# Kernel tuning notes

Measured on AMD Instinct MI355X. Metric: run time of the kernel, lower is better.

The kernel has to match this reference:

```python
import jax, jax.numpy as jnp
import numpy as np

NSAMPLE = 16
BN_EPS = 1e-5


def setup_inputs() -> dict:
    key = jax.random.key(0)
    k1, k2, k3, k4, k5, k6 = jax.random.split(key, 6)
    B, N, Cin, Cout = 8, 8192, 64, 128
    xyz = jax.random.normal(k1, (B, N, 3), dtype=jnp.float32)
    feature = jax.random.normal(k2, (B, N, Cin), dtype=jnp.float32)
    W = jax.random.normal(k3, (Cin, Cout), dtype=jnp.float32) * 0.05
    b = jax.random.normal(k4, (Cout,), dtype=jnp.float32) * 0.01
    gamma = 1.0 + 0.1 * jax.random.normal(k5, (Cout,), dtype=jnp.float32)
    beta = 0.1 * jax.random.normal(k6, (Cout,), dtype=jnp.float32)
    return {"xyz": xyz, "feature": feature, "W": W, "b": b,
            "gamma": gamma, "beta": beta, "npoint": 2048}


def farthest_point_sample(xyz, npoint):
    # xyz: [B, N, 3] -> centroids: [B, npoint] int32
    B, N, _ = xyz.shape
    dist0 = jnp.full((B, N), 1e10, dtype=xyz.dtype)
    far0 = jnp.zeros((B,), dtype=jnp.int32)  # deterministic seed point (torch uses randint)

    def step(carry, _):
        distance, farthest = carry
        centroid = jnp.take_along_axis(xyz, farthest[:, None, None], axis=1)  # [B,1,3]
        d = jnp.sum((xyz - centroid) ** 2, axis=-1)  # [B,N]
        distance = jnp.minimum(distance, d)
        new_far = jnp.argmax(distance, axis=-1).astype(jnp.int32)
        return (distance, new_far), farthest

    (_, _), cents = jax.lax.scan(step, (dist0, far0), None, length=npoint)
    return cents.T  # [B, npoint]


def index_points(points, idx):
    # points: [B, N, C]; idx: [B, ...] -> [B, ..., C]
    B = points.shape[0]
    C = points.shape[-1]
    flat = idx.reshape(B, -1)
    out = jnp.take_along_axis(points, flat[..., None], axis=1)  # [B, M, C]
    return out.reshape(idx.shape + (C,))


def knn_point(nsample, xyz, new_xyz):
    # squared distances [B, npoint, N], then nsample smallest
    sqr = (-2.0 * jnp.einsum('bmc,bnc->bmn', new_xyz, xyz)
           + jnp.sum(new_xyz ** 2, -1)[..., None]
           + jnp.sum(xyz ** 2, -1)[:, None, :])
    _, idx = jax.lax.top_k(-sqr, nsample)
    return idx  # [B, npoint, nsample]


def reference(xyz, feature, W, b, gamma, beta, npoint):
    B = xyz.shape[0]
    new_xyz_idx = farthest_point_sample(xyz, npoint)          # [B, npoint]
    new_xyz = index_points(xyz, new_xyz_idx)                  # [B, npoint, 3]
    idx = knn_point(NSAMPLE, xyz, new_xyz)                    # [B, npoint, K]
    grouped_feature = index_points(feature, idx)              # [B, npoint, K, Cin]

    # pointwise MLP: Linear -> BatchNorm (batch stats, per out-channel) -> ReLU
    h = jnp.einsum('bnkc,cd->bnkd', grouped_feature, W) + b   # [B, npoint, K, Cout]
    mean = jnp.mean(h, axis=(0, 1, 2))
    var = jnp.mean((h - mean) ** 2, axis=(0, 1, 2))           # biased, as torch BN
    h = gamma * (h - mean) * jax.lax.rsqrt(var + BN_EPS) + beta
    h = jax.nn.relu(h)

    new_feature = jnp.max(h, axis=2)                          # [B, npoint, Cout]
    return new_xyz, new_feature
```

## Files before the change

kernel.cpp:

```cpp
#include <hip/hip_runtime.h>

typedef unsigned long long u64;
typedef unsigned int u32;
typedef float f32x2 __attribute__((ext_vector_type(2)));

constexpr int BATCH  = 8;
constexpr int NPTS   = 8192;
constexpr int CIN    = 64;
constexpr int COUT   = 128;
constexpr int NPOINT = 2048;
constexpr int KNN    = 16;

__global__ __launch_bounds__(256) void pp_kernel(const float* __restrict__ xyz,
                                                 float* __restrict__ pp) {
  int i = blockIdx.x * 256 + threadIdx.x;
  float x = xyz[i * 3 + 0], y = xyz[i * 3 + 1], z = xyz[i * 3 + 2];
  pp[i] = __fadd_rn(__fadd_rn(__fmul_rn(x, x), __fmul_rn(y, y)), __fmul_rn(z, z));
}

constexpr int FPS_T = 256;
constexpr int FPS_PAIRS = NPTS / FPS_T / 2;

#define DPP_LVL(CTRL)                                                          \
  {                                                                            \
    u32 hi_o = (u32)__builtin_amdgcn_update_dpp((int)khi, (int)khi, (CTRL),    \
                                                0xf, 0xf, false);              \
    u32 lo_o = (u32)__builtin_amdgcn_update_dpp((int)klo, (int)klo, (CTRL),    \
                                                0xf, 0xf, false);              \
    bool gt = (hi_o > khi) || ((hi_o == khi) && (lo_o > klo));                 \
    khi = gt ? hi_o : khi;                                                     \
    klo = gt ? lo_o : klo;                                                     \
  }

__global__ __launch_bounds__(256) void fps_kernel(const float* __restrict__ xyz,
                                                  float* __restrict__ out_xyz) {
#pragma clang fp contract(off)
  __shared__ float4 sP[NPTS];
  __shared__ u64 sKey[2][4];
  const int b = blockIdx.x;
  const int t = threadIdx.x;
  const int lane = t & 63;
  const int wv = t >> 6;
  const float* xb = xyz + (size_t)b * NPTS * 3;
  f32x2 px2[FPS_PAIRS], py2[FPS_PAIRS], pz2[FPS_PAIRS], pd2[FPS_PAIRS];
#pragma unroll
  for (int jp = 0; jp < FPS_PAIRS; ++jp) {
    int p0 = t + (2 * jp) * FPS_T;
    int p1 = t + (2 * jp + 1) * FPS_T;
    float x0 = xb[p0 * 3 + 0], y0 = xb[p0 * 3 + 1], z0 = xb[p0 * 3 + 2];
    float x1 = xb[p1 * 3 + 0], y1 = xb[p1 * 3 + 1], z1 = xb[p1 * 3 + 2];
    px2[jp] = (f32x2){x0, x1};
    py2[jp] = (f32x2){y0, y1};
    pz2[jp] = (f32x2){z0, z1};
    pd2[jp] = (f32x2){1e10f, 1e10f};
    sP[p0] = make_float4(x0, y0, z0, 0.f);
    sP[p1] = make_float4(x1, y1, z1, 0.f);
  }
  float cx = xb[0], cy = xb[1], cz = xb[2];
  float* outx = out_xyz + (size_t)b * NPOINT * 3;
  __syncthreads();
  for (int it = 0; it < NPOINT; ++it) {
    if (t == 0) {
      outx[it * 3 + 0] = cx; outx[it * 3 + 1] = cy; outx[it * 3 + 2] = cz;
    }
    const f32x2 cx2 = {cx, cx}, cy2 = {cy, cy}, cz2 = {cz, cz};
    float bd = -1.0f;
    int bj = 0;
#pragma unroll
    for (int jp = 0; jp < FPS_PAIRS; ++jp) {
      f32x2 dx = px2[jp] - cx2;
      f32x2 dy = py2[jp] - cy2;
      f32x2 dz = pz2[jp] - cz2;
      f32x2 d = (dx * dx + dy * dy) + dz * dz;
      f32x2 nd = __builtin_elementwise_min(pd2[jp], d);
      pd2[jp] = nd;
      if (nd.x > bd) { bd = nd.x; bj = 2 * jp; }
      if (nd.y > bd) { bd = nd.y; bj = 2 * jp + 1; }
    }
    const int bi0 = t + bj * FPS_T;
    u32 khi = __float_as_uint(bd);
    u32 klo = (u32)(8191 - bi0);
    DPP_LVL(0x111)
    DPP_LVL(0x112)
    DPP_LVL(0x114)
    DPP_LVL(0x118)
    DPP_LVL(0x142)
    DPP_LVL(0x143)
    const int par = it & 1;
    if (lane == 63) sKey[par][wv] = ((u64)khi << 32) | klo;
    __syncthreads();
    u64 k0 = sKey[par][0];
    u64 k1 = sKey[par][1];
    u64 k2 = sKey[par][2];
    u64 k3 = sKey[par][3];
    if (k1 > k0) k0 = k1;
    if (k3 > k2) k2 = k3;
    if (k2 > k0) k0 = k2;
    const int bi = 8191 - (int)(u32)(k0 & 0xFFFFFFFFu);
    float4 c4 = sP[bi];
    cx = c4.x; cy = c4.y; cz = c4.z;
  }
}

__global__ __launch_bounds__(512) void knn_kernel(const float* __restrict__ xyz,
                                                  const float* __restrict__ pp,
                                                  const float* __restrict__ new_xyz,
                                                  int* __restrict__ knn_idx) {
  __shared__ u64 smem[8192];
  const int tid = threadIdx.x;
  const int lane = tid & 63;
  const int wv = __builtin_amdgcn_readfirstlane(tid >> 6);
  const int bid = blockIdx.x;
  const int b = bid >> 5;
  const int qbase = (bid & 31) * 64;
  const int q = qbase + lane;
  const float* xb = xyz + (size_t)b * NPTS * 3;
  const float* ppb = pp + (size_t)b * NPTS;
  const float* nq = new_xyz + ((size_t)b * NPOINT + q) * 3;
  float qx = nq[0], qy = nq[1], qz = nq[2];
  float qq = __fadd_rn(__fadd_rn(__fmul_rn(qx, qx), __fmul_rn(qy, qy)),
                       __fmul_rn(qz, qz));

  u64 L[16];
#pragma unroll
  for (int s = 0; s < 16; ++s) L[s] = 0xFF800000FFFFFFFFULL;
  float cmax = __uint_as_float(0x7F800000u);
  int cnt = 0;

  auto flushfn = [&]() {
#pragma unroll
    for (int e = 0; e < 8; ++e) {
      if (e < cnt) {
        u64 key = smem[tid * 9 + e];
        if (key < L[15]) {
#pragma unroll
          for (int s = 15; s >= 1; --s)
            L[s] = (key < L[s - 1]) ? L[s - 1] : ((key < L[s]) ? key : L[s]);
          L[0] = (key < L[0]) ? key : L[0];
        }
      }
    }
    cnt = 0;
    u32 hb = (u32)(L[15] >> 32);
    hb ^= (hb >= 0x80000000u) ? 0x80000000u : 0xFFFFFFFFu;
    cmax = __uint_as_float(hb);
  };

  const int base = wv * 1024;
#pragma unroll 8
  for (int i = 0; i < 1024; ++i) {
    const int pidx = base + i;
    float ptx = xb[pidx * 3 + 0], pty = xb[pidx * 3 + 1], ptz = xb[pidx * 3 + 2];
    float pv = ppb[pidx];
    float dot = __fadd_rn(__fadd_rn(__fmul_rn(qx, ptx), __fmul_rn(qy, pty)),
                          __fmul_rn(qz, ptz));
    float d = __fadd_rn(__fadd_rn(__fmul_rn(-2.0f, dot), qq), pv);
    if (d <= cmax) {
      u32 xb32 = __float_as_uint(d);
      xb32 ^= ((int)xb32 < 0) ? 0xFFFFFFFFu : 0x80000000u;
      smem[tid * 9 + cnt] = ((u64)xb32 << 32) | (u32)pidx;
      ++cnt;
    }
    if (__any(cnt >= 8)) flushfn();
  }
  flushfn();
  __syncthreads();
#pragma unroll
  for (int s = 0; s < 16; ++s) smem[tid * 16 + s] = L[s];
  __syncthreads();
  if (tid < 64) {
    u64 h[8]; int pos[8];
#pragma unroll
    for (int w = 0; w < 8; ++w) { h[w] = smem[(w * 64 + tid) * 16]; pos[w] = 1; }
    int outv[16];
#pragma unroll
    for (int r = 0; r < 16; ++r) {
      u64 mv = h[0]; int mw = 0;
#pragma unroll
      for (int w = 1; w < 8; ++w) {
        if (h[w] < mv) { mv = h[w]; mw = w; }
      }
      outv[r] = (int)(mv & 0xFFFFFFFFULL);
#pragma unroll
      for (int w = 0; w < 8; ++w) {
        if (w == mw) {
          h[w] = (pos[w] < 16) ? smem[(w * 64 + tid) * 16 + pos[w]]
                               : 0xFFFFFFFFFFFFFFFFULL;
          pos[w]++;
        }
      }
    }
    int* dst = knn_idx + ((size_t)b * NPOINT + qbase + tid) * KNN;
#pragma unroll
    for (int r = 0; r < 16; r += 4)
      *(int4*)(dst + r) = make_int4(outv[r], outv[r + 1], outv[r + 2], outv[r + 3]);
  }
}

__global__ __launch_bounds__(256) void stats_kernel(const float* __restrict__ feature,
                                                    const float* __restrict__ Wm,
                                                    const float* __restrict__ bias,
                                                    const int* __restrict__ knn_idx,
                                                    double* __restrict__ stats) {
  __shared__ float s_part[256];
  const int tid = threadIdx.x;
  const int lane = tid & 63;
  const int wv = tid >> 6;
  const int tbase = blockIdx.x * 256 + tid;
  for (int chunk = 0; chunk < 4; ++chunk) {
    const int c0 = chunk * 32;
    float V[64];
#pragma unroll
    for (int j = 0; j < 64; ++j) V[j] = 0.f;
    for (int rr = 0; rr < 4; ++rr) {
      const int row = tbase + rr * 65536;
      const int bb = row >> 15;
      const int nbr = knn_idx[row];
      const float4* fp = (const float4*)(feature + ((size_t)bb * NPTS + nbr) * CIN);
      float acc[32];
#pragma unroll
      for (int j = 0; j < 32; ++j) acc[j] = bias[c0 + j];
      for (int cb = 0; cb < 8; ++cb) {
        float4 fa = fp[cb * 2 + 0], fb2 = fp[cb * 2 + 1];
        float fr[8] = {fa.x, fa.y, fa.z, fa.w, fb2.x, fb2.y, fb2.z, fb2.w};
#pragma unroll
        for (int cc = 0; cc < 8; ++cc) {
          const int c = cb * 8 + cc;
#pragma unroll
          for (int j = 0; j < 32; ++j)
            acc[j] = fmaf(fr[cc], Wm[c * COUT + c0 + j], acc[j]);
        }
      }
#pragma unroll
      for (int j = 0; j < 32; ++j) {
        V[j] += acc[j];
        V[32 + j] = fmaf(acc[j], acc[j], V[32 + j]);
      }
    }
#pragma unroll
    for (int o = 32; o >= 1; o >>= 1) {
      const bool hi = (lane & o) != 0;
#pragma unroll
      for (int j = 0; j < o; ++j) {
        float keep = hi ? V[o + j] : V[j];
        float send = hi ? V[j] : V[o + j];
        V[j] = keep + __shfl_xor(send, o);
      }
    }
    s_part[wv * 64 + lane] = V[0];
    __syncthreads();
    if (tid < 64) {
      float tot = s_part[tid] + s_part[64 + tid] + s_part[128 + tid] + s_part[192 + tid];
      int addr = (tid < 32) ? (c0 + tid) : (COUT + c0 + (tid - 32));
      atomicAdd(stats + addr, (double)tot);
    }
    __syncthreads();
  }
}

__global__ __launch_bounds__(256) void apply_kernel(const float* __restrict__ feature,
                                                    const float* __restrict__ Wm,
                                                    const float* __restrict__ bias,
                                                    const float* __restrict__ gamma,
                                                    const float* __restrict__ beta,
                                                    const int* __restrict__ knn_idx,
                                                    const double* __restrict__ stats,
                                                    float* __restrict__ out_feat) {
  __shared__ float s_sc[COUT], s_sh[COUT];
  const int tid = threadIdx.x;
  if (tid < COUT) {
    const double inv_n = 1.0 / (double)(BATCH * NPOINT * KNN);
    double mean = stats[tid] * inv_n;
    double var = stats[COUT + tid] * inv_n - mean * mean;
    double s = (double)gamma[tid] / sqrt(var + 1e-5);
    s_sc[tid] = (float)s;
    s_sh[tid] = (float)((double)beta[tid] - mean * s);
  }
  __syncthreads();
  const int k = tid & 15;
  const int qg = blockIdx.x * 16 + (tid >> 4);
  const int bb = qg >> 11;
  const int nbr = knn_idx[qg * KNN + k];
  const float4* fp = (const float4*)(feature + ((size_t)bb * NPTS + nbr) * CIN);
  float* outp = out_feat + (size_t)qg * COUT;
  for (int chunk = 0; chunk < 4; ++chunk) {
    const int c0 = chunk * 32;
    float acc[32];
#pragma unroll
    for (int j = 0; j < 32; ++j) acc[j] = bias[c0 + j];
    for (int cb = 0; cb < 8; ++cb) {
      float4 fa = fp[cb * 2 + 0], fb2 = fp[cb * 2 + 1];
      float fr[8] = {fa.x, fa.y, fa.z, fa.w, fb2.x, fb2.y, fb2.z, fb2.w};
#pragma unroll
      for (int cc = 0; cc < 8; ++cc) {
        const int c = cb * 8 + cc;
#pragma unroll
        for (int j = 0; j < 32; ++j)
          acc[j] = fmaf(fr[cc], Wm[c * COUT + c0 + j], acc[j]);
      }
    }
#pragma unroll
    for (int j = 0; j < 32; ++j) {
      float n = fmaxf(fmaf(acc[j], s_sc[c0 + j], s_sh[c0 + j]), 0.0f);
#pragma unroll
      for (int off = 8; off >= 1; off >>= 1)
        n = fmaxf(n, __shfl_xor(n, off));
      acc[j] = n;
    }
    if (k == 0) {
#pragma unroll
      for (int j = 0; j < 32; j += 4)
        *(float4*)(outp + c0 + j) = make_float4(acc[j], acc[j + 1], acc[j + 2], acc[j + 3]);
    }
  }
}

extern "C" void kernel_launch(void* const* d_in, const int* in_sizes, int n_in,
                              void* d_out, int out_size, void* d_ws, size_t ws_size,
                              hipStream_t stream) {
  (void)in_sizes; (void)n_in; (void)out_size; (void)ws_size;
  const float* xyz = (const float*)d_in[0];
  const float* feature = (const float*)d_in[1];
  const float* Wm = (const float*)d_in[2];
  const float* bias = (const float*)d_in[3];
  const float* gamma = (const float*)d_in[4];
  const float* beta = (const float*)d_in[5];

  float* out_xyz = (float*)d_out;
  float* out_feat = (float*)d_out + (size_t)BATCH * NPOINT * 3;

  int* knn_idx = (int*)d_ws;
  double* stats = (double*)((char*)d_ws + (1 << 20));
  float* pp = (float*)((char*)d_ws + (1 << 20) + 4096);

  pp_kernel<<<dim3(256), dim3(256), 0, stream>>>(xyz, pp);
  fps_kernel<<<dim3(BATCH), dim3(FPS_T), 0, stream>>>(xyz, out_xyz);
  knn_kernel<<<dim3(256), dim3(512), 0, stream>>>(xyz, pp, out_xyz, knn_idx);
  (void)hipMemsetAsync(stats, 0, 2 * COUT * sizeof(double), stream);
  stats_kernel<<<dim3(256), dim3(256), 0, stream>>>(feature, Wm, bias, knn_idx, stats);
  apply_kernel<<<dim3(1024), dim3(256), 0, stream>>>(feature, Wm, bias, gamma, beta,
                                                     knn_idx, stats, out_feat);
}
```

Measured before the change: 2.406 ms.

## Streamline FPS inner loop with packed asm, fmax reduction, and LDS-staged output

```diff
diff --git a/kernel.cpp b/kernel.cpp
--- a/kernel.cpp
+++ b/kernel.cpp
@@ -20,6 +20,23 @@
 
 constexpr int FPS_T = 256;
 constexpr int FPS_PAIRS = NPTS / FPS_T / 2;
+
+static __device__ __forceinline__ f32x2 pk_sub(f32x2 a, f32x2 b) {
+  f32x2 r;
+  asm("v_pk_add_f32 %0, %1, %2 neg_lo:[0,1] neg_hi:[0,1]"
+      : "=v"(r) : "v"(a), "v"(b));
+  return r;
+}
+static __device__ __forceinline__ f32x2 pk_mul(f32x2 a, f32x2 b) {
+  f32x2 r;
+  asm("v_pk_mul_f32 %0, %1, %2" : "=v"(r) : "v"(a), "v"(b));
+  return r;
+}
+static __device__ __forceinline__ f32x2 pk_add(f32x2 a, f32x2 b) {
+  f32x2 r;
+  asm("v_pk_add_f32 %0, %1, %2" : "=v"(r) : "v"(a), "v"(b));
+  return r;
+}
 
 #define DPP_LVL(CTRL)                                                          \
   {                                                                            \
@@ -34,8 +51,8 @@
 
 __global__ __launch_bounds__(256) void fps_kernel(const float* __restrict__ xyz,
                                                   float* __restrict__ out_xyz) {
-#pragma clang fp contract(off)
   __shared__ float4 sP[NPTS];
+  __shared__ float sOut[NPOINT * 3];
   __shared__ u64 sKey[2][4];
   const int b = blockIdx.x;
   const int t = threadIdx.x;
@@ -61,21 +78,25 @@
   __syncthreads();
   for (int it = 0; it < NPOINT; ++it) {
     if (t == 0) {
-      outx[it * 3 + 0] = cx; outx[it * 3 + 1] = cy; outx[it * 3 + 2] = cz;
+      sOut[it * 3 + 0] = cx; sOut[it * 3 + 1] = cy; sOut[it * 3 + 2] = cz;
     }
     const f32x2 cx2 = {cx, cx}, cy2 = {cy, cy}, cz2 = {cz, cz};
     float bd = -1.0f;
-    int bj = 0;
 #pragma unroll
     for (int jp = 0; jp < FPS_PAIRS; ++jp) {
-      f32x2 dx = px2[jp] - cx2;
-      f32x2 dy = py2[jp] - cy2;
-      f32x2 dz = pz2[jp] - cz2;
-      f32x2 d = (dx * dx + dy * dy) + dz * dz;
+      f32x2 dx = pk_sub(px2[jp], cx2);
+      f32x2 dy = pk_sub(py2[jp], cy2);
+      f32x2 dz = pk_sub(pz2[jp], cz2);
+      f32x2 d = pk_add(pk_add(pk_mul(dx, dx), pk_mul(dy, dy)), pk_mul(dz, dz));
       f32x2 nd = __builtin_elementwise_min(pd2[jp], d);
       pd2[jp] = nd;
-      if (nd.x > bd) { bd = nd.x; bj = 2 * jp; }
-      if (nd.y > bd) { bd = nd.y; bj = 2 * jp + 1; }
+      bd = fmaxf(fmaxf(bd, nd.x), nd.y);
+    }
+    int bj = 0;
+#pragma unroll
+    for (int jp = FPS_PAIRS - 1; jp >= 0; --jp) {
+      if (pd2[jp].y == bd) bj = 2 * jp + 1;
+      if (pd2[jp].x == bd) bj = 2 * jp;
     }
     const int bi0 = t + bj * FPS_T;
     u32 khi = __float_as_uint(bd);
@@ -100,6 +121,8 @@
     float4 c4 = sP[bi];
     cx = c4.x; cy = c4.y; cz = c4.z;
   }
+  __syncthreads();
+  for (int i = t; i < NPOINT * 3; i += FPS_T) outx[i] = sOut[i];
 }
 
 __global__ __launch_bounds__(512) void knn_kernel(const float* __restrict__ xyz,
```

Result: slower. 2.543 ms (+5.7%).
